# Kernel optimization log

Measured on AMD Instinct MI355X. Metric: run time of the kernel, lower is better.

## Reference

```python
import jax, jax.numpy as jnp
import numpy as np

N, E = 50000, 800000
NODE_DIM, EDGE_DIM = 96, 64
IN_DIM = 2 * NODE_DIM + EDGE_DIM  # 256


def setup_inputs() -> dict:
    key = jax.random.key(0)
    k = jax.random.split(key, 7)
    h = jax.random.normal(k[0], (N, NODE_DIM), dtype=jnp.float32)
    edge_index = jax.random.randint(k[1], (2, E), 0, N, dtype=jnp.int64)
    edge_attr = jax.random.normal(k[2], (E, EDGE_DIM), dtype=jnp.float32)
    # Linear params (PyTorch default-ish scale)
    s = 1.0 / np.sqrt(IN_DIM)
    W_e = jax.random.uniform(k[3], (IN_DIM, NODE_DIM), jnp.float32, -s, s)
    b_e = jax.random.uniform(k[4], (NODE_DIM,), jnp.float32, -s, s)
    W_n = jax.random.uniform(k[5], (IN_DIM, NODE_DIM), jnp.float32, -s, s)
    b_n = jax.random.uniform(k[6], (NODE_DIM,), jnp.float32, -s, s)
    return {"h": h, "edge_index": edge_index, "edge_attr": edge_attr,
            "W_e": W_e, "b_e": b_e, "W_n": W_n, "b_n": b_n}


def reference(h, edge_index, edge_attr, W_e, b_e, W_n, b_n):
    src, dst = edge_index[0], edge_index[1]
    concat = jnp.concatenate([h[src], h[dst], edge_attr], axis=-1)  # [E, 256]
    gates = jax.nn.sigmoid(concat @ W_e + b_e)                      # [E, node_dim]
    messages = jax.nn.softplus(concat @ W_n + b_n)                  # [E, node_dim]
    gated = gates * messages
    n = h.shape[0]
    h_new = jax.ops.segment_sum(gated, dst, num_segments=n)         # [N, node_dim]
    edge_count = jax.ops.segment_sum(jnp.ones((dst.shape[0],), h.dtype), dst, num_segments=n)
    edge_count = jnp.clip(edge_count, 1.0, None)[:, None]
    return h + h_new / edge_count
```

## Files before the change

### kernel.cpp

```cpp
#include <hip/hip_runtime.h>
#include <hip/hip_bf16.h>


#define NODE_DIM 96
#define EDGE_DIM 64
#define IN_DIM   256
#define NT_TILES 12
#define KT_TILES 8

typedef float  f32x4  __attribute__((ext_vector_type(4)));
typedef __bf16 bf16x8 __attribute__((ext_vector_type(8)));

__device__ __forceinline__ unsigned short bf16rne(float f) {
    unsigned int u = __float_as_uint(f);
    u += 0x7FFFu + ((u >> 16) & 1u);
    return (unsigned short)(u >> 16);
}

__global__ void pack_w_kernel(const float* __restrict__ We,
                              const float* __restrict__ Wn,
                              unsigned short* __restrict__ bpack) {
    int t = blockIdx.x * blockDim.x + threadIdx.x;
    if (t >= KT_TILES * NT_TILES * 64) return;
    int tile = t >> 6, lane = t & 63;
    int kt = tile / NT_TILES, nt = tile % NT_TILES;
    const float* W = (nt < 6) ? We : Wn;
    int n  = (nt % 6) * 16 + (lane & 15);
    int k0 = kt * 32 + (lane >> 4) * 8;
    union { unsigned short u[8]; uint4 v; } tmp;
#pragma unroll
    for (int j = 0; j < 8; ++j) tmp.u[j] = bf16rne(W[(k0 + j) * NODE_DIM + n]);
    *(uint4*)(bpack + (size_t)t * 8) = tmp.v;
}

__global__ void cvt_h_kernel(const float* __restrict__ h,
                             unsigned short* __restrict__ hb, int total8) {
    int i = blockIdx.x * 256 + threadIdx.x;
    if (i >= total8) return;
    const float4 v0 = ((const float4*)h)[i * 2];
    const float4 v1 = ((const float4*)h)[i * 2 + 1];
    union { unsigned short u[8]; uint4 v; } p;
    p.u[0] = bf16rne(v0.x); p.u[1] = bf16rne(v0.y);
    p.u[2] = bf16rne(v0.z); p.u[3] = bf16rne(v0.w);
    p.u[4] = bf16rne(v1.x); p.u[5] = bf16rne(v1.y);
    p.u[6] = bf16rne(v1.z); p.u[7] = bf16rne(v1.w);
    ((uint4*)hb)[i] = p.v;
}

__global__ __launch_bounds__(256, 3)
void gemm_atomic_kernel(const unsigned short* __restrict__ hb,
                        const int*   __restrict__ eidx,
                        const float* __restrict__ ea,
                        const unsigned short* __restrict__ bpack,
                        const float* __restrict__ be,
                        const float* __restrict__ bn,
                        float* __restrict__ hnew,
                        float* __restrict__ cnt,
                        int E) {
    const int tid  = threadIdx.x;
    const int wave = tid >> 6, lane = tid & 63;
    const int m    = lane & 15;
    const int quad = lane >> 4;
    const int base = blockIdx.x * 128 + wave * 32;

    const unsigned short* hsq[2];
    const unsigned short* hdq[2];
    const float*          epq[2];
    int dstv[2];
#pragma unroll
    for (int mt = 0; mt < 2; ++mt) {
        int e  = base + mt * 16 + m;
        int eg = (e < E) ? e : (E - 1);
        int src = eidx[eg];
        int dst = eidx[E + eg];
        dstv[mt] = dst;
        hsq[mt] = hb + (size_t)src * NODE_DIM + quad * 8;
        hdq[mt] = hb + (size_t)dst * NODE_DIM + quad * 8;
        epq[mt] = ea + (size_t)eg  * EDGE_DIM + quad * 8;
        if (quad == 0 && e < E) unsafeAtomicAdd(cnt + dst, 1.0f);
    }
    const unsigned short* bl = bpack + lane * 8;

    f32x4 acc[2][NT_TILES];
#pragma unroll
    for (int mt = 0; mt < 2; ++mt)
#pragma unroll
        for (int nt = 0; nt < NT_TILES; ++nt) acc[mt][nt] = (f32x4){0.f, 0.f, 0.f, 0.f};

#pragma unroll
    for (int kt = 0; kt < KT_TILES; ++kt) {
        bf16x8 A[2];
#pragma unroll
        for (int mt = 0; mt < 2; ++mt) {
            if (kt < 3) {
                A[mt] = *(const bf16x8*)(hsq[mt] + kt * 32);
            } else if (kt < 6) {
                A[mt] = *(const bf16x8*)(hdq[mt] + (kt - 3) * 32);
            } else {
                const float4 v0 = *(const float4*)(epq[mt] + (kt - 6) * 32);
                const float4 v1 = *(const float4*)(epq[mt] + (kt - 6) * 32 + 4);
                union { unsigned short u[8]; bf16x8 b; } t;
                t.u[0] = bf16rne(v0.x); t.u[1] = bf16rne(v0.y);
                t.u[2] = bf16rne(v0.z); t.u[3] = bf16rne(v0.w);
                t.u[4] = bf16rne(v1.x); t.u[5] = bf16rne(v1.y);
                t.u[6] = bf16rne(v1.z); t.u[7] = bf16rne(v1.w);
                A[mt] = t.b;
            }
        }
#pragma unroll
        for (int nt = 0; nt < NT_TILES; ++nt) {
            bf16x8 bfrag = *(const bf16x8*)(bl + (kt * NT_TILES + nt) * 512);
            acc[0][nt] = __builtin_amdgcn_mfma_f32_16x16x32_bf16(A[0], bfrag, acc[0][nt], 0, 0, 0);
            acc[1][nt] = __builtin_amdgcn_mfma_f32_16x16x32_bf16(A[1], bfrag, acc[1][nt], 0, 0, 0);
        }
    }

#pragma unroll
    for (int mt = 0; mt < 2; ++mt) {
#pragma unroll
        for (int r = 0; r < 4; ++r) {
            const int ee = base + mt * 16 + quad * 4 + r;
            const int d  = __shfl(dstv[mt], quad * 4 + r, 64);
            if (ee >= E) continue;
            float* hrow = hnew + (size_t)d * NODE_DIM;
#pragma unroll
            for (int nt = 0; nt < 6; ++nt) {
                const int col = nt * 16 + m;
                float g  = acc[mt][nt][r]     + be[col];
                float mm = acc[mt][nt + 6][r] + bn[col];
                float gate = 1.0f / (1.0f + __expf(-g));
                float sp   = fmaxf(mm, 0.0f) + __logf(1.0f + __expf(-fabsf(mm)));
                unsafeAtomicAdd(hrow + col, gate * sp);
            }
        }
    }
}

__global__ void finalize_kernel(const float* __restrict__ h,
                                const float* __restrict__ hnew,
                                const float* __restrict__ cnt,
                                float* __restrict__ out,
                                int total4) {
    int i = blockIdx.x * blockDim.x + threadIdx.x;
    if (i >= total4) return;
    int n = i / 24;
    float inv = 1.0f / fmaxf(cnt[n], 1.0f);
    float4 hv = ((const float4*)h)[i];
    float4 av = ((const float4*)hnew)[i];
    float4 o = {hv.x + av.x * inv, hv.y + av.y * inv, hv.z + av.z * inv, hv.w + av.w * inv};
    ((float4*)out)[i] = o;
}

extern "C" void kernel_launch(void* const* d_in, const int* in_sizes, int n_in,
                              void* d_out, int out_size, void* d_ws, size_t ws_size,
                              hipStream_t stream) {
    const float* h   = (const float*)d_in[0];
    const int*   ei  = (const int*)  d_in[1];
    const float* ea  = (const float*)d_in[2];
    const float* We  = (const float*)d_in[3];
    const float* be  = (const float*)d_in[4];
    const float* Wn  = (const float*)d_in[5];
    const float* bn  = (const float*)d_in[6];

    const int N = in_sizes[0] / NODE_DIM;
    const int E = in_sizes[2] / EDGE_DIM;
    char* ws = (char*)d_ws;

    size_t off = 0;
    auto take = [&](size_t bytes) { size_t o = off; off = (off + bytes + 511) & ~(size_t)511; return o; };
    const size_t O_BPACK = take((size_t)KT_TILES * NT_TILES * 64 * 16);
    const size_t O_CNT   = take((size_t)N * 4);
    const size_t O_HNEW  = take((size_t)N * NODE_DIM * 4);
    const size_t O_HB    = take((size_t)N * NODE_DIM * 2);
    (void)ws_size;

    unsigned short* bpack = (unsigned short*)(ws + O_BPACK);
    float* cnt  = (float*)(ws + O_CNT);
    float* hnew = (float*)(ws + O_HNEW);
    unsigned short* hb = (unsigned short*)(ws + O_HB);

    hipMemsetAsync(ws + O_CNT, 0, O_HB - O_CNT, stream);

    pack_w_kernel<<<(KT_TILES * NT_TILES * 64 + 255) / 256, 256, 0, stream>>>(We, Wn, bpack);

    const int total8 = N * NODE_DIM / 8;
    cvt_h_kernel<<<(total8 + 255) / 256, 256, 0, stream>>>(h, hb, total8);

    gemm_atomic_kernel<<<(E + 127) / 128, 256, 0, stream>>>(hb, ei, ea, bpack, be, bn, hnew, cnt, E);

    const int total4 = N * (NODE_DIM / 4);
    finalize_kernel<<<(total4 + 255) / 256, 256, 0, stream>>>(h, hnew, cnt, (float*)d_out, total4);
}
```

Before: 698.1 us.

## Sort edges by destination via counting sort and pre-reduce atomics per row

Adds a histogram, three-pass scan and scatter that bucket edges by destination node. The GEMM kernel then reads edges in sorted order and sums consecutive same-destination rows in registers before issuing atomics. Degree counts now come from CSR offsets instead of float atomics. The goal is fewer contended atomic adds into h_new. The cost is five extra kernel launches, scattered gathers of edge_attr through the permutation, and more workspace. With an average degree of about 16 and 4 rows per lane group, each atomic merges at most a few rows.

```diff
diff --git a/kernel.cpp b/kernel.cpp
--- a/kernel.cpp
+++ b/kernel.cpp
@@ -47,15 +47,91 @@
     ((uint4*)hb)[i] = p.v;
 }
 
+__global__ void hist_kernel(const int* __restrict__ eidx, unsigned* __restrict__ deg, int E) {
+    int e = blockIdx.x * 256 + threadIdx.x;
+    if (e < E) atomicAdd(deg + eidx[E + e], 1u);
+}
+
+__device__ __forceinline__ unsigned block_excl_scan_256(unsigned v, int tid,
+                                                        unsigned* wsum, unsigned* wpre,
+                                                        unsigned* total) {
+    int lane = tid & 63, w = tid >> 6;
+    unsigned inc = v;
+#pragma unroll
+    for (int o = 1; o < 64; o <<= 1) {
+        unsigned t = __shfl_up(inc, o, 64);
+        if (lane >= o) inc += t;
+    }
+    if (lane == 63) wsum[w] = inc;
+    __syncthreads();
+    if (tid == 0) {
+        unsigned s = 0;
+#pragma unroll
+        for (int k = 0; k < 4; ++k) { wpre[k] = s; s += wsum[k]; }
+        *total = s;
+    }
+    __syncthreads();
+    return inc - v + wpre[w];
+}
+
+__global__ void scan_block_kernel(const unsigned* __restrict__ deg,
+                                  unsigned* __restrict__ scanned,
+                                  unsigned* __restrict__ blocksum, int N) {
+    __shared__ unsigned wsum[4], wpre[4], total;
+    int tid = threadIdx.x;
+    int i = blockIdx.x * 256 + tid;
+    unsigned v = (i < N) ? deg[i] : 0u;
+    unsigned excl = block_excl_scan_256(v, tid, wsum, wpre, &total);
+    if (i < N) scanned[i] = excl;
+    if (tid == 0) blocksum[blockIdx.x] = total;
+}
+
+__global__ void scan_sums_kernel(const unsigned* __restrict__ blocksum,
+                                 unsigned* __restrict__ blockpref, int NB) {
+    __shared__ unsigned wsum[4], wpre[4], total;
+    int tid = threadIdx.x;
+    unsigned v = (tid < NB) ? blocksum[tid] : 0u;
+    unsigned excl = block_excl_scan_256(v, tid, wsum, wpre, &total);
+    if (tid < NB) blockpref[tid] = excl;
+}
+
+__global__ void scan_finalize_kernel(const unsigned* __restrict__ scanned,
+                                     const unsigned* __restrict__ blockpref,
+                                     unsigned* __restrict__ offsets,
+                                     unsigned* __restrict__ cursor, int N, int E) {
+    int i = blockIdx.x * 256 + threadIdx.x;
+    if (i < N) {
+        unsigned o = scanned[i] + blockpref[i >> 8];
+        offsets[i] = o;
+        cursor[i]  = o;
+    }
+    if (i == 0) offsets[N] = (unsigned)E;
+}
+
+__global__ void scatter_kernel(const int* __restrict__ eidx,
+                               unsigned* __restrict__ cursor,
+                               int2* __restrict__ s_se,
+                               int*  __restrict__ s_d,
+                               int E) {
+    int e = blockIdx.x * 256 + threadIdx.x;
+    if (e < E) {
+        int s = eidx[e];
+        int d = eidx[E + e];
+        unsigned pos = atomicAdd(cursor + d, 1u);
+        s_se[pos] = make_int2(s, e);
+        s_d[pos]  = d;
+    }
+}
+
 __global__ __launch_bounds__(256, 3)
-void gemm_atomic_kernel(const unsigned short* __restrict__ hb,
-                        const int*   __restrict__ eidx,
+void gemm_sorted_kernel(const unsigned short* __restrict__ hb,
+                        const int2* __restrict__ s_se,
+                        const int*  __restrict__ s_d,
                         const float* __restrict__ ea,
                         const unsigned short* __restrict__ bpack,
                         const float* __restrict__ be,
                         const float* __restrict__ bn,
                         float* __restrict__ hnew,
-                        float* __restrict__ cnt,
                         int E) {
     const int tid  = threadIdx.x;
     const int wave = tid >> 6, lane = tid & 63;
@@ -69,15 +145,14 @@
     int dstv[2];
 #pragma unroll
     for (int mt = 0; mt < 2; ++mt) {
-        int e  = base + mt * 16 + m;
-        int eg = (e < E) ? e : (E - 1);
-        int src = eidx[eg];
-        int dst = eidx[E + eg];
+        int r  = base + mt * 16 + m;
+        int rg = (r < E) ? r : (E - 1);
+        int2 se = s_se[rg];
+        int dst = s_d[rg];
         dstv[mt] = dst;
-        hsq[mt] = hb + (size_t)src * NODE_DIM + quad * 8;
-        hdq[mt] = hb + (size_t)dst * NODE_DIM + quad * 8;
-        epq[mt] = ea + (size_t)eg  * EDGE_DIM + quad * 8;
-        if (quad == 0 && e < E) unsafeAtomicAdd(cnt + dst, 1.0f);
+        hsq[mt] = hb + (size_t)se.x * NODE_DIM + quad * 8;
+        hdq[mt] = hb + (size_t)dst  * NODE_DIM + quad * 8;
+        epq[mt] = ea + (size_t)se.y * EDGE_DIM + quad * 8;
     }
     const unsigned short* bl = bpack + lane * 8;
 
@@ -117,12 +192,14 @@
 
 #pragma unroll
     for (int mt = 0; mt < 2; ++mt) {
+        int dprev = -1;
+        float s[6];
 #pragma unroll
         for (int r = 0; r < 4; ++r) {
             const int ee = base + mt * 16 + quad * 4 + r;
             const int d  = __shfl(dstv[mt], quad * 4 + r, 64);
             if (ee >= E) continue;
-            float* hrow = hnew + (size_t)d * NODE_DIM;
+            float v[6];
 #pragma unroll
             for (int nt = 0; nt < 6; ++nt) {
                 const int col = nt * 16 + m;
@@ -130,21 +207,40 @@
                 float mm = acc[mt][nt + 6][r] + bn[col];
                 float gate = 1.0f / (1.0f + __expf(-g));
                 float sp   = fmaxf(mm, 0.0f) + __logf(1.0f + __expf(-fabsf(mm)));
-                unsafeAtomicAdd(hrow + col, gate * sp);
+                v[nt] = gate * sp;
+            }
+            if (d != dprev) {
+                if (dprev >= 0) {
+                    float* hrow = hnew + (size_t)dprev * NODE_DIM + m;
+#pragma unroll
+                    for (int nt = 0; nt < 6; ++nt) unsafeAtomicAdd(hrow + nt * 16, s[nt]);
+                }
+#pragma unroll
+                for (int nt = 0; nt < 6; ++nt) s[nt] = v[nt];
+                dprev = d;
+            } else {
+#pragma unroll
+                for (int nt = 0; nt < 6; ++nt) s[nt] += v[nt];
             }
         }
+        if (dprev >= 0) {
+            float* hrow = hnew + (size_t)dprev * NODE_DIM + m;
+#pragma unroll
+            for (int nt = 0; nt < 6; ++nt) unsafeAtomicAdd(hrow + nt * 16, s[nt]);
+        }
     }
 }
 
 __global__ void finalize_kernel(const float* __restrict__ h,
                                 const float* __restrict__ hnew,
-                                const float* __restrict__ cnt,
+                                const unsigned* __restrict__ offsets,
                                 float* __restrict__ out,
                                 int total4) {
     int i = blockIdx.x * blockDim.x + threadIdx.x;
     if (i >= total4) return;
     int n = i / 24;
-    float inv = 1.0f / fmaxf(cnt[n], 1.0f);
+    unsigned deg = offsets[n + 1] - offsets[n];
+    float inv = 1.0f / (float)(deg > 0u ? deg : 1u);
     float4 hv = ((const float4*)h)[i];
     float4 av = ((const float4*)hnew)[i];
     float4 o = {hv.x + av.x * inv, hv.y + av.y * inv, hv.z + av.z * inv, hv.w + av.w * inv};
@@ -169,25 +265,48 @@
     size_t off = 0;
     auto take = [&](size_t bytes) { size_t o = off; off = (off + bytes + 511) & ~(size_t)511; return o; };
     const size_t O_BPACK = take((size_t)KT_TILES * NT_TILES * 64 * 16);
-    const size_t O_CNT   = take((size_t)N * 4);
+    const size_t O_DEG   = take((size_t)N * 4);
     const size_t O_HNEW  = take((size_t)N * NODE_DIM * 4);
+    const size_t O_MEMSET_END = off;
+    const size_t O_SCAN  = take((size_t)N * 4);
+    const size_t O_BSUM  = take(1024);
+    const size_t O_BPREF = take(1024);
+    const size_t O_OFFS  = take((size_t)(N + 1) * 4);
+    const size_t O_CURS  = take((size_t)N * 4);
+    const size_t O_SSE   = take((size_t)E * 8);
+    const size_t O_SD    = take((size_t)E * 4);
     const size_t O_HB    = take((size_t)N * NODE_DIM * 2);
     (void)ws_size;
 
     unsigned short* bpack = (unsigned short*)(ws + O_BPACK);
-    float* cnt  = (float*)(ws + O_CNT);
-    float* hnew = (float*)(ws + O_HNEW);
+    unsigned* deg   = (unsigned*)(ws + O_DEG);
+    float*    hnew  = (float*)(ws + O_HNEW);
+    unsigned* scn   = (unsigned*)(ws + O_SCAN);
+    unsigned* bsum  = (unsigned*)(ws + O_BSUM);
+    unsigned* bpref = (unsigned*)(ws + O_BPREF);
+    unsigned* offs  = (unsigned*)(ws + O_OFFS);
+    unsigned* curs  = (unsigned*)(ws + O_CURS);
+    int2*     s_se  = (int2*)(ws + O_SSE);
+    int*      s_d   = (int*)(ws + O_SD);
     unsigned short* hb = (unsigned short*)(ws + O_HB);
 
-    hipMemsetAsync(ws + O_CNT, 0, O_HB - O_CNT, stream);
+    hipMemsetAsync(ws + O_DEG, 0, O_MEMSET_END - O_DEG, stream);
 
     pack_w_kernel<<<(KT_TILES * NT_TILES * 64 + 255) / 256, 256, 0, stream>>>(We, Wn, bpack);
 
     const int total8 = N * NODE_DIM / 8;
     cvt_h_kernel<<<(total8 + 255) / 256, 256, 0, stream>>>(h, hb, total8);
 
-    gemm_atomic_kernel<<<(E + 127) / 128, 256, 0, stream>>>(hb, ei, ea, bpack, be, bn, hnew, cnt, E);
+    const int NB = (N + 255) / 256;
+    hist_kernel<<<(E + 255) / 256, 256, 0, stream>>>(ei, deg, E);
+    scan_block_kernel<<<NB, 256, 0, stream>>>(deg, scn, bsum, N);
+    scan_sums_kernel<<<1, 256, 0, stream>>>(bsum, bpref, NB);
+    scan_finalize_kernel<<<NB, 256, 0, stream>>>(scn, bpref, offs, curs, N, E);
+    scatter_kernel<<<(E + 255) / 256, 256, 0, stream>>>(ei, curs, s_se, s_d, E);
+
+    gemm_sorted_kernel<<<(E + 127) / 128, 256, 0, stream>>>(hb, s_se, s_d, ea, bpack,
+                                                            be, bn, hnew, E);
 
     const int total4 = N * (NODE_DIM / 4);
-    finalize_kernel<<<(total4 + 255) / 256, 256, 0, stream>>>(h, hnew, cnt, (float*)d_out, total4);
-}
+    finalize_kernel<<<(total4 + 255) / 256, 256, 0, stream>>>(h, hnew, offs, (float*)d_out, total4);
+}
```

Result: faster. 645.7 us (-7.5%).
